# Performance work log

Hardware: AMD Instinct MI355X
Metric: run time of the kernel (lower is better)

The kernel has to match this reference:

```python
import jax, jax.numpy as jnp
import numpy as np

N = 100000
E = 1600000
IN_CH = 256
HID = 48
OUT_CH = 4
BN_EPS = 1e-5


def setup_inputs() -> dict:
    key = jax.random.key(0)
    ks = jax.random.split(key, 16)
    x = jax.random.normal(ks[0], (N, IN_CH), dtype=jnp.float32)
    edge_index = jax.random.randint(ks[1], (2, E), 0, N, dtype=jnp.int64)
    s = lambda k, shape, fan: jax.random.normal(k, shape, dtype=jnp.float32) / np.sqrt(fan)
    return {
        "x": x,
        "edge_index": edge_index,
        # conv1 (SAGEConv: lin_l on aggregated neighbors w/ bias, lin_r on root, no bias)
        "w1l": s(ks[2], (HID, IN_CH), IN_CH),
        "b1": jnp.zeros((HID,), jnp.float32),
        "w1r": s(ks[3], (HID, IN_CH), IN_CH),
        # bn1 (inference mode: running stats)
        "g1": jnp.ones((HID,), jnp.float32),
        "be1": jnp.zeros((HID,), jnp.float32),
        "rm1": 0.1 * jax.random.normal(ks[4], (HID,), dtype=jnp.float32),
        "rv1": jnp.ones((HID,), jnp.float32) + 0.1 * jax.random.uniform(ks[5], (HID,)),
        # conv2
        "w2l": s(ks[6], (HID, HID), HID),
        "b2": jnp.zeros((HID,), jnp.float32),
        "w2r": s(ks[7], (HID, HID), HID),
        # bn2
        "g2": jnp.ones((HID,), jnp.float32),
        "be2": jnp.zeros((HID,), jnp.float32),
        "rm2": 0.1 * jax.random.normal(ks[8], (HID,), dtype=jnp.float32),
        "rv2": jnp.ones((HID,), jnp.float32) + 0.1 * jax.random.uniform(ks[9], (HID,)),
        # output linear
        "wo": s(ks[10], (OUT_CH, HID), HID),
        "bo": jnp.zeros((OUT_CH,), jnp.float32),
    }


def _sage_conv(h, src, dst, wl, bl, wr, n_nodes):
    # mean-aggregate neighbor features: gather x[src], scatter-sum onto dst, divide by degree
    msgs = h[src]                                             # [E, F] irregular gather
    agg = jax.ops.segment_sum(msgs, dst, num_segments=n_nodes)  # [N, F]
    deg = jax.ops.segment_sum(jnp.ones((src.shape[0],), h.dtype), dst, num_segments=n_nodes)
    mean = agg / jnp.maximum(deg, 1.0)[:, None]
    return mean @ wl.T + bl + h @ wr.T


def _bn_eval(h, g, b, rm, rv):
    return (h - rm) * (g * jax.lax.rsqrt(rv + BN_EPS)) + b


def reference(x, edge_index, w1l, b1, w1r, g1, be1, rm1, rv1,
              w2l, b2, w2r, g2, be2, rm2, rv2, wo, bo):
    src, dst = edge_index[0], edge_index[1]
    n = x.shape[0]
    h = jax.nn.relu(_bn_eval(_sage_conv(x, src, dst, w1l, b1, w1r, n), g1, be1, rm1, rv1))
    h = jax.nn.relu(_bn_eval(_sage_conv(h, src, dst, w2l, b2, w2r, n), g2, be2, rm2, rv2))
    return h @ wo.T + bo
```

## Files before the change

kernel.cpp:

```cpp
#include <hip/hip_runtime.h>
#include <hip/hip_bf16.h>

#define N_NODES 100000
#define N_EDGES 1600000
#define IN_CH   256
#define BN_EPS  1e-5f
#define SCAN_NB 98

typedef __attribute__((ext_vector_type(8))) short bf16x8;
typedef __attribute__((ext_vector_type(4))) float f32x4;
typedef __attribute__((ext_vector_type(4))) int   i32x4;

__device__ inline unsigned f2bf(float x) {
    unsigned u = __float_as_uint(x);
    return (u + 0x7fffu + ((u >> 16) & 1u)) >> 16;
}
__device__ inline unsigned pk2(float x, float y) {
    return f2bf(x) | (f2bf(y) << 16);
}
__device__ inline bf16x8 pack8(float4 a, float4 b) {
    i32x4 r;
    r.x = (int)pk2(a.x, a.y); r.y = (int)pk2(a.z, a.w);
    r.z = (int)pk2(b.x, b.y); r.w = (int)pk2(b.z, b.w);
    return __builtin_bit_cast(bf16x8, r);
}
__device__ inline float lo16(unsigned u) { return __uint_as_float(u << 16); }
__device__ inline float hi16(unsigned u) { return __uint_as_float(u & 0xffff0000u); }

__global__ void hist_kernel(const int* __restrict__ ei, int* __restrict__ cnt) {
    int e = blockIdx.x * blockDim.x + threadIdx.x;
    if (e >= N_EDGES) return;
    int dst = ei[N_EDGES + e];
    if ((unsigned)dst < N_NODES) atomicAdd(&cnt[dst], 1);
}

__global__ __launch_bounds__(256) void scan_k1(const int* __restrict__ cnt, int* __restrict__ bsum) {
    __shared__ int lds[256];
    int b = blockIdx.x, t = threadIdx.x;
    int i0 = b * 1024 + t * 4;
    int s = 0;
#pragma unroll
    for (int j = 0; j < 4; j++) { int i = i0 + j; if (i < N_NODES) s += cnt[i]; }
    lds[t] = s; __syncthreads();
    for (int o = 128; o; o >>= 1) { if (t < o) lds[t] += lds[t + o]; __syncthreads(); }
    if (t == 0) bsum[b] = lds[0];
}

__global__ void scan_k2(const int* __restrict__ bsum, int* __restrict__ bex, int nb) {
    __shared__ int lds[128];
    int t = threadIdx.x;
    int v = (t < nb) ? bsum[t] : 0;
    lds[t] = v; __syncthreads();
    for (int o = 1; o < 128; o <<= 1) {
        int u = (t >= o) ? lds[t - o] : 0;
        __syncthreads();
        lds[t] += u;
        __syncthreads();
    }
    if (t < nb) bex[t] = lds[t] - v;
}

__global__ __launch_bounds__(256) void scan_k3(const int* __restrict__ cnt, const int* __restrict__ bex,
                                               int* __restrict__ off, int* __restrict__ cur) {
    __shared__ int lds[256];
    int b = blockIdx.x, t = threadIdx.x;
    int i0 = b * 1024 + t * 4;
    int c[4]; int s = 0;
#pragma unroll
    for (int j = 0; j < 4; j++) { int i = i0 + j; c[j] = (i < N_NODES) ? cnt[i] : 0; s += c[j]; }
    lds[t] = s; __syncthreads();
    for (int o = 1; o < 256; o <<= 1) {
        int u = (t >= o) ? lds[t - o] : 0;
        __syncthreads();
        lds[t] += u;
        __syncthreads();
    }
    int ex = lds[t] - s + bex[b];
#pragma unroll
    for (int j = 0; j < 4; j++) {
        int i = i0 + j;
        if (i < N_NODES) { off[i] = ex; cur[i] = ex; ex += c[j]; }
    }
}

__global__ void scatter_kernel(const int* __restrict__ ei, int* __restrict__ cur,
                               int* __restrict__ csr) {
    int e = blockIdx.x * blockDim.x + threadIdx.x;
    if (e >= N_EDGES) return;
    int src = ei[e];
    int dst = ei[N_EDGES + e];
    if ((unsigned)src >= N_NODES || (unsigned)dst >= N_NODES) return;
    int pos = atomicAdd(&cur[dst], 1);
    csr[pos] = src;
}

__global__ __launch_bounds__(256) void gemm1_mfma(const float* __restrict__ in,
        const float* __restrict__ W0, const float* __restrict__ W1,
        __hip_bfloat16* __restrict__ P, float* __restrict__ R) {
    __shared__ bf16x8 wlds[8 * 6 * 64];
    int tid = threadIdx.x;
    for (int s = tid; s < 8 * 6 * 64; s += 256) {
        int lane = s & 63, tile = (s >> 6) % 6, kstep = s / 384;
        int c = tile * 16 + (lane & 15);
        int k0 = kstep * 32 + (lane >> 4) * 8;
        const float* Wp = (c < 48) ? &W0[(size_t)c * IN_CH] : &W1[(size_t)(c - 48) * IN_CH];
        float4 a = *(const float4*)&Wp[k0];
        float4 b = *(const float4*)&Wp[k0 + 4];
        wlds[s] = pack8(a, b);
    }
    __syncthreads();

    int w = tid >> 6, lane = tid & 63;
    int lr = lane & 15, kq = lane >> 4;
    int rbase = blockIdx.x * 128 + w * 32;
    f32x4 acc[2][6] = {};

    for (int kstep = 0; kstep < 8; kstep++) {
        int kb = kstep * 32 + kq * 8;
        bf16x8 afr[2] = {};
#pragma unroll
        for (int mt = 0; mt < 2; mt++) {
            int row = rbase + mt * 16 + lr;
            if (row < N_NODES) {
                const float* ip = &in[(size_t)row * IN_CH + kb];
                afr[mt] = pack8(*(const float4*)ip, *(const float4*)(ip + 4));
            }
        }
        bf16x8 bfr[6];
#pragma unroll
        for (int t = 0; t < 6; t++) bfr[t] = wlds[(kstep * 6 + t) * 64 + lane];
#pragma unroll
        for (int t = 0; t < 6; t++)
#pragma unroll
            for (int mt = 0; mt < 2; mt++)
                acc[mt][t] = __builtin_amdgcn_mfma_f32_16x16x32_bf16(afr[mt], bfr[t], acc[mt][t], 0, 0, 0);
    }
#pragma unroll
    for (int mt = 0; mt < 2; mt++)
#pragma unroll
        for (int t = 0; t < 6; t++)
#pragma unroll
            for (int j = 0; j < 4; j++) {
                int row = rbase + mt * 16 + kq * 4 + j;
                if (row < N_NODES) {
                    float v = acc[mt][t][j];
                    int col = t * 16 + lr;
                    if (t < 3) P[(size_t)row * 48 + col] = __float2bfloat16(v);
                    else       R[(size_t)row * 48 + (col - 48)] = v;
                }
            }
}

__global__ __launch_bounds__(256) void gemm2_mfma(const __hip_bfloat16* __restrict__ inb,
        const float* __restrict__ W0, const float* __restrict__ W1,
        __hip_bfloat16* __restrict__ P, float* __restrict__ R) {
    __shared__ bf16x8 wlds[2 * 6 * 64];
    int tid = threadIdx.x;
    for (int s = tid; s < 2 * 6 * 64; s += 256) {
        int lane = s & 63, tile = (s >> 6) % 6, kstep = s / 384;
        int c = tile * 16 + (lane & 15);
        int k0 = kstep * 32 + (lane >> 4) * 8;
        const float* Wp = (c < 48) ? &W0[(size_t)c * 48] : &W1[(size_t)(c - 48) * 48];
        float v[8];
#pragma unroll
        for (int j = 0; j < 8; j++) { int k = k0 + j; v[j] = (k < 48) ? Wp[k] : 0.f; }
        wlds[s] = pack8(make_float4(v[0], v[1], v[2], v[3]), make_float4(v[4], v[5], v[6], v[7]));
    }
    __syncthreads();

    int w = tid >> 6, lane = tid & 63;
    int lr = lane & 15, kq = lane >> 4;
    int rbase = blockIdx.x * 128 + w * 32;
    f32x4 acc[2][6] = {};

    for (int kstep = 0; kstep < 2; kstep++) {
        int kb = kstep * 32 + kq * 8;
        bf16x8 afr[2] = {};
#pragma unroll
        for (int mt = 0; mt < 2; mt++) {
            int row = rbase + mt * 16 + lr;
            if (row < N_NODES)
                afr[mt] = *(const bf16x8*)&inb[(size_t)row * 64 + kb];
        }
        bf16x8 bfr[6];
#pragma unroll
        for (int t = 0; t < 6; t++) bfr[t] = wlds[(kstep * 6 + t) * 64 + lane];
#pragma unroll
        for (int t = 0; t < 6; t++)
#pragma unroll
            for (int mt = 0; mt < 2; mt++)
                acc[mt][t] = __builtin_amdgcn_mfma_f32_16x16x32_bf16(afr[mt], bfr[t], acc[mt][t], 0, 0, 0);
    }
#pragma unroll
    for (int mt = 0; mt < 2; mt++)
#pragma unroll
        for (int t = 0; t < 6; t++)
#pragma unroll
            for (int j = 0; j < 4; j++) {
                int row = rbase + mt * 16 + kq * 4 + j;
                if (row < N_NODES) {
                    float v = acc[mt][t][j];
                    int col = t * 16 + lr;
                    if (t < 3) P[(size_t)row * 48 + col] = __float2bfloat16(v);
                    else       R[(size_t)row * 48 + (col - 48)] = v;
                }
            }
}

__global__ __launch_bounds__(256) void agg_csr_b16(const int* __restrict__ off, const int* __restrict__ cnt,
                                                   const int* __restrict__ csr,
                                                   const unsigned* __restrict__ P32,
                                                   float* __restrict__ agg) {
    int t = blockIdx.x * blockDim.x + threadIdx.x;
    int node = t >> 3, l = t & 7;
    if (node >= N_NODES) return;
    int s = off[node], len = cnt[node];
    float a0 = 0.f, a1 = 0.f, a2 = 0.f, a3 = 0.f, a4 = 0.f, a5 = 0.f;
    int i = 0;
    for (; i + 4 <= len; i += 4) {
        int sx[4];
#pragma unroll
        for (int q = 0; q < 4; q++) sx[q] = csr[s + i + q];
        unsigned uu[4][3];
#pragma unroll
        for (int q = 0; q < 4; q++) {
            const unsigned* p = P32 + (size_t)sx[q] * 24 + l;
            uu[q][0] = p[0]; uu[q][1] = p[8]; uu[q][2] = p[16];
        }
#pragma unroll
        for (int q = 0; q < 4; q++) {
            a0 += lo16(uu[q][0]); a1 += hi16(uu[q][0]);
            a2 += lo16(uu[q][1]); a3 += hi16(uu[q][1]);
            a4 += lo16(uu[q][2]); a5 += hi16(uu[q][2]);
        }
    }
    for (; i < len; i++) {
        const unsigned* p = P32 + (size_t)csr[s + i] * 24 + l;
        unsigned u0 = p[0], u1 = p[8], u2 = p[16];
        a0 += lo16(u0); a1 += hi16(u0);
        a2 += lo16(u1); a3 += hi16(u1);
        a4 += lo16(u2); a5 += hi16(u2);
    }
    size_t base = (size_t)node * 48;
    *(float2*)&agg[base +  0 + 2 * l] = make_float2(a0, a1);
    *(float2*)&agg[base + 16 + 2 * l] = make_float2(a2, a3);
    *(float2*)&agg[base + 32 + 2 * l] = make_float2(a4, a5);
}

__global__ void post1_kernel(const float* __restrict__ agg, const int* __restrict__ cnt,
                             const float* __restrict__ R,
                             const float* __restrict__ b,  const float* __restrict__ g,
                             const float* __restrict__ be, const float* __restrict__ rm,
                             const float* __restrict__ rv, __hip_bfloat16* __restrict__ h) {
    int t = blockIdx.x * blockDim.x + threadIdx.x;
    if (t >= N_NODES * 48) return;
    int n = t / 48, j = t % 48;
    float mean = agg[t] / fmaxf((float)cnt[n], 1.0f);
    float v = mean + b[j] + R[t];
    v = (v - rm[j]) * (g[j] * rsqrtf(rv[j] + BN_EPS)) + be[j];
    h[(size_t)n * 64 + j] = __float2bfloat16(fmaxf(v, 0.0f));
}

__global__ void out_kernel(const float* __restrict__ agg, const int* __restrict__ cnt,
                           const float* __restrict__ R,
                           const float* __restrict__ b2, const float* __restrict__ g2,
                           const float* __restrict__ be2, const float* __restrict__ rm2,
                           const float* __restrict__ rv2,
                           const float* __restrict__ wo, const float* __restrict__ bo,
                           float* __restrict__ out) {
    int t = blockIdx.x * blockDim.x + threadIdx.x;
    int node = t >> 4, l = t & 15;
    if (node >= N_NODES) return;
    float dg = fmaxf((float)cnt[node], 1.0f);
    float p0 = 0.f, p1 = 0.f, p2 = 0.f, p3 = 0.f;
#pragma unroll
    for (int q = 0; q < 3; q++) {
        int j = l + q * 16;
        float v = agg[(size_t)node * 48 + j] / dg + b2[j] + R[(size_t)node * 48 + j];
        v = (v - rm2[j]) * (g2[j] * rsqrtf(rv2[j] + BN_EPS)) + be2[j];
        v = fmaxf(v, 0.f);
        p0 = fmaf(v, wo[0 * 48 + j], p0);
        p1 = fmaf(v, wo[1 * 48 + j], p1);
        p2 = fmaf(v, wo[2 * 48 + j], p2);
        p3 = fmaf(v, wo[3 * 48 + j], p3);
    }
#pragma unroll
    for (int offm = 8; offm; offm >>= 1) {
        p0 += __shfl_down(p0, offm, 16);
        p1 += __shfl_down(p1, offm, 16);
        p2 += __shfl_down(p2, offm, 16);
        p3 += __shfl_down(p3, offm, 16);
    }
    if (l == 0) {
        float4 o = make_float4(p0 + bo[0], p1 + bo[1], p2 + bo[2], p3 + bo[3]);
        *(float4*)&out[(size_t)node * 4] = o;
    }
}

extern "C" void kernel_launch(void* const* d_in, const int* in_sizes, int n_in,
                              void* d_out, int out_size, void* d_ws, size_t ws_size,
                              hipStream_t stream) {
    const float* x   = (const float*)d_in[0];
    const int*   ei  = (const int*)d_in[1];
    const float* w1l = (const float*)d_in[2];
    const float* b1  = (const float*)d_in[3];
    const float* w1r = (const float*)d_in[4];
    const float* g1  = (const float*)d_in[5];
    const float* be1 = (const float*)d_in[6];
    const float* rm1 = (const float*)d_in[7];
    const float* rv1 = (const float*)d_in[8];
    const float* w2l = (const float*)d_in[9];
    const float* b2  = (const float*)d_in[10];
    const float* w2r = (const float*)d_in[11];
    const float* g2  = (const float*)d_in[12];
    const float* be2 = (const float*)d_in[13];
    const float* rm2 = (const float*)d_in[14];
    const float* rv2 = (const float*)d_in[15];
    const float* wo  = (const float*)d_in[16];
    const float* bo  = (const float*)d_in[17];
    float* out = (float*)d_out;

    char* w = (char*)d_ws;
    float*           Rbuf = (float*)w;                       w += (size_t)N_NODES * 48 * 4;
    float*           AGG  = (float*)w;                       w += (size_t)N_NODES * 48 * 4;
    __hip_bfloat16*  P    = (__hip_bfloat16*)w;              w += (size_t)N_NODES * 48 * 2;
    __hip_bfloat16*  H1   = (__hip_bfloat16*)w;              w += (size_t)N_NODES * 64 * 2;
    int*             CNT  = (int*)w;                         w += (size_t)N_NODES * 4;
    int*             OFF  = (int*)w;                         w += (size_t)N_NODES * 4;
    int*             CUR  = (int*)w;                         w += (size_t)N_NODES * 4;
    int*             BSUM = (int*)w;                         w += 128 * 4;
    int*             BEX  = (int*)w;                         w += 128 * 4;
    int*             CSR  = (int*)w;

    (void)hipMemsetAsync(CNT, 0, N_NODES * sizeof(int), stream);
    (void)hipMemsetAsync(H1, 0, (size_t)N_NODES * 64 * 2, stream);

    hist_kernel<<<(N_EDGES + 255) / 256, 256, 0, stream>>>(ei, CNT);
    scan_k1<<<SCAN_NB, 256, 0, stream>>>(CNT, BSUM);
    scan_k2<<<1, 128, 0, stream>>>(BSUM, BEX, SCAN_NB);
    scan_k3<<<SCAN_NB, 256, 0, stream>>>(CNT, BEX, OFF, CUR);
    scatter_kernel<<<(N_EDGES + 255) / 256, 256, 0, stream>>>(ei, CUR, CSR);

    gemm1_mfma<<<(N_NODES + 127) / 128, 256, 0, stream>>>(x, w1l, w1r, P, Rbuf);
    agg_csr_b16<<<(N_NODES * 8 + 255) / 256, 256, 0, stream>>>(OFF, CNT, CSR, (const unsigned*)P, AGG);
    post1_kernel<<<(N_NODES * 48 + 255) / 256, 256, 0, stream>>>(AGG, CNT, Rbuf,
                                                                 b1, g1, be1, rm1, rv1, H1);

    gemm2_mfma<<<(N_NODES + 127) / 128, 256, 0, stream>>>(H1, w2l, w2r, P, Rbuf);
    agg_csr_b16<<<(N_NODES * 8 + 255) / 256, 256, 0, stream>>>(OFF, CNT, CSR, (const unsigned*)P, AGG);
    out_kernel<<<(N_NODES * 16 + 255) / 256, 256, 0, stream>>>(AGG, CNT, Rbuf,
                                                               b2, g2, be2, rm2, rv2,
                                                               wo, bo, out);
}
```

Before: 516.5 us.

## Partition histogram and CSR scatter atomics by destination range across blocks

Replaces the one-thread-per-edge histogram and scatter kernels with partitioned versions. Blockidx selects one of 8 destination-node ranges and each block strides over all edges, doing atomics only for destinations in its range. The intent is to keep each block's atomic targets inside a smaller working set (likely one per XCD/L2) and cut contention and cache thrashing. In exchange the edge list is read 8 times.

```diff
diff --git a/kernel.cpp b/kernel.cpp
--- a/kernel.cpp
+++ b/kernel.cpp
@@ -6,6 +6,9 @@
 #define IN_CH   256
 #define BN_EPS  1e-5f
 #define SCAN_NB 98
+#define NPART   8
+#define PART_SZ 12500
+#define NGRP    128
 
 typedef __attribute__((ext_vector_type(8))) short bf16x8;
 typedef __attribute__((ext_vector_type(4))) float f32x4;
@@ -27,11 +30,31 @@
 __device__ inline float lo16(unsigned u) { return __uint_as_float(u << 16); }
 __device__ inline float hi16(unsigned u) { return __uint_as_float(u & 0xffff0000u); }
 
-__global__ void hist_kernel(const int* __restrict__ ei, int* __restrict__ cnt) {
-    int e = blockIdx.x * blockDim.x + threadIdx.x;
-    if (e >= N_EDGES) return;
-    int dst = ei[N_EDGES + e];
-    if ((unsigned)dst < N_NODES) atomicAdd(&cnt[dst], 1);
+__global__ __launch_bounds__(256) void hist_part(const int* __restrict__ ei, int* __restrict__ cnt) {
+    int p = blockIdx.x & (NPART - 1);
+    int g = blockIdx.x >> 3;
+    int lo = p * PART_SZ, hi = lo + PART_SZ;
+    for (int e = g * 256 + (int)threadIdx.x; e < N_EDGES; e += NGRP * 256) {
+        int dst = ei[N_EDGES + e];
+        if (dst >= lo && dst < hi) atomicAdd(&cnt[dst], 1);
+    }
+}
+
+__global__ __launch_bounds__(256) void scatter_part(const int* __restrict__ ei, int* __restrict__ cur,
+                                                    int* __restrict__ csr) {
+    int p = blockIdx.x & (NPART - 1);
+    int g = blockIdx.x >> 3;
+    int lo = p * PART_SZ, hi = lo + PART_SZ;
+    for (int e = g * 256 + (int)threadIdx.x; e < N_EDGES; e += NGRP * 256) {
+        int dst = ei[N_EDGES + e];
+        if (dst >= lo && dst < hi) {
+            int src = ei[e];
+            if ((unsigned)src < N_NODES) {
+                int pos = atomicAdd(&cur[dst], 1);
+                csr[pos] = src;
+            }
+        }
+    }
 }
 
 __global__ __launch_bounds__(256) void scan_k1(const int* __restrict__ cnt, int* __restrict__ bsum) {
@@ -81,17 +104,6 @@
         int i = i0 + j;
         if (i < N_NODES) { off[i] = ex; cur[i] = ex; ex += c[j]; }
     }
-}
-
-__global__ void scatter_kernel(const int* __restrict__ ei, int* __restrict__ cur,
-                               int* __restrict__ csr) {
-    int e = blockIdx.x * blockDim.x + threadIdx.x;
-    if (e >= N_EDGES) return;
-    int src = ei[e];
-    int dst = ei[N_EDGES + e];
-    if ((unsigned)src >= N_NODES || (unsigned)dst >= N_NODES) return;
-    int pos = atomicAdd(&cur[dst], 1);
-    csr[pos] = src;
 }
 
 __global__ __launch_bounds__(256) void gemm1_mfma(const float* __restrict__ in,
@@ -335,11 +347,11 @@
     (void)hipMemsetAsync(CNT, 0, N_NODES * sizeof(int), stream);
     (void)hipMemsetAsync(H1, 0, (size_t)N_NODES * 64 * 2, stream);
 
-    hist_kernel<<<(N_EDGES + 255) / 256, 256, 0, stream>>>(ei, CNT);
+    hist_part<<<NPART * NGRP, 256, 0, stream>>>(ei, CNT);
     scan_k1<<<SCAN_NB, 256, 0, stream>>>(CNT, BSUM);
     scan_k2<<<1, 128, 0, stream>>>(BSUM, BEX, SCAN_NB);
     scan_k3<<<SCAN_NB, 256, 0, stream>>>(CNT, BEX, OFF, CUR);
-    scatter_kernel<<<(N_EDGES + 255) / 256, 256, 0, stream>>>(ei, CUR, CSR);
+    scatter_part<<<NPART * NGRP, 256, 0, stream>>>(ei, CUR, CSR);
 
     gemm1_mfma<<<(N_NODES + 127) / 128, 256, 0, stream>>>(x, w1l, w1r, P, Rbuf);
     agg_csr_b16<<<(N_NODES * 8 + 255) / 256, 256, 0, stream>>>(OFF, CNT, CSR, (const unsigned*)P, AGG);
```

After: 483.1 us. 6.5% less time.
